# Optimization experiments

Measured on AMD Instinct MI355X. Metric: run time of the kernel, lower is better.

## Reference

```python
import jax, jax.numpy as jnp
import numpy as np

B, OBS, H, A, E = 131072, 194, 64, 5, 3  # batch, obs dim, hidden, max_action_dim, n event types


def setup_inputs() -> dict:
    key = jax.random.key(0)
    ks = jax.random.split(key, 16)
    s = lambda k, shape, std=0.1: (jax.random.normal(k, shape, dtype=jnp.float32) * std)
    return {
        "x": jax.random.normal(ks[0], (B, OBS), dtype=jnp.float32),
        "action": jax.random.randint(ks[1], (B,), 0, A),
        "W1": s(ks[2], (OBS, H)), "b1": jnp.zeros((H,), jnp.float32),
        "W2": s(ks[3], (H, H)),   "b2": jnp.zeros((H,), jnp.float32),
        "Wh": s(ks[4], (E, H, A), 0.01), "bh": jnp.zeros((E, A), jnp.float32),
        "Wc1": s(ks[5], (OBS, H)), "bc1": jnp.zeros((H,), jnp.float32),
        "Wc2": s(ks[6], (H, H)),   "bc2": jnp.zeros((H,), jnp.float32),
        "Wc3": s(ks[7], (H, 1)),   "bc3": jnp.zeros((1,), jnp.float32),
    }


def reference(x, action, W1, b1, W2, b2, Wh, bh, Wc1, bc1, Wc2, bc2, Wc3, bc3):
    # shared trunk
    feat = jnp.tanh(jnp.tanh(x @ W1 + b1) @ W2 + b2)          # [B, H]
    # route each sample to one of E heads via argmax of first 3 obs dims
    ev = jnp.argmax(x[:, :E], axis=1)                          # [B] int
    all_logits = jnp.einsum('bh,eha->bea', feat, Wh) + bh      # [B, E, A]
    logits = jnp.take_along_axis(
        all_logits, jnp.broadcast_to(ev[:, None, None], (x.shape[0], 1, A)), axis=1
    )[:, 0]                                                    # [B, A]
    logp_all = jax.nn.log_softmax(logits, axis=-1)             # [B, A]
    logp = jnp.take_along_axis(logp_all, action[:, None], axis=1)[:, 0]  # [B]
    entropy = -jnp.sum(jnp.exp(logp_all) * logp_all, axis=-1)  # [B]
    # critic
    value = jnp.tanh(jnp.tanh(x @ Wc1 + bc1) @ Wc2 + bc2) @ Wc3 + bc3    # [B, 1]
    return action, logp, entropy, value
```

## Files before the change

### kernel.cpp

```cpp
#include <hip/hip_runtime.h>
#include <hip/hip_bf16.h>

constexpr int Bt  = 131072;
constexpr int OBS = 194;
constexpr int Hd  = 64;
constexpr int NT  = 256;
constexpr int MT  = 128;
constexpr int HS  = 72;
constexpr int LS  = 18;

constexpr int W1B_OFF  = 0;
constexpr int WC1B_OFF = 28672;
constexpr int W2B_OFF  = 57344;
constexpr int WC2B_OFF = 65536;
constexpr int WHB_OFF  = 73728;
constexpr int WS_SHORTS = 74752;

typedef short bf8   __attribute__((ext_vector_type(8)));
typedef float f32x4 __attribute__((ext_vector_type(4)));

__device__ __forceinline__ short f2bs(float f) {
    union { __hip_bfloat16 h; short s; } u;
    u.h = __float2bfloat16(f);
    return u.s;
}
__device__ __forceinline__ float bs2f(short s) {
    union { short s; __hip_bfloat16 h; } u;
    u.s = s;
    return __bfloat162float(u.h);
}
__device__ __forceinline__ float fast_tanh(float v) {
    v = fminf(fmaxf(v, -15.f), 15.f);
    float e = __expf(2.f * v);
    return (e - 1.f) * __builtin_amdgcn_rcpf(e + 1.f);
}

__global__ void __launch_bounds__(256) prep(
    const float* __restrict__ W1, const float* __restrict__ W2,
    const float* __restrict__ Wh, const float* __restrict__ Wc1,
    const float* __restrict__ Wc2, const float* __restrict__ Wc3,
    short* __restrict__ ws)
{
    const int gid = blockIdx.x * 256 + threadIdx.x;
    const int gsz = gridDim.x * 256;

    for (int i = gid; i < 28672; i += gsz) {
        int j = i & 7, l = (i >> 3) & 63, nt = (i >> 9) & 3, kb = i >> 11;
        int k = kb * 32 + ((l >> 4) << 3) + j;
        int n = nt * 16 + (l & 15);
        short v1 = 0, v2 = 0;
        if (k < OBS) {
            v1 = f2bs(W1[k * 64 + n]);
            v2 = f2bs(Wc1[k * 64 + n]);
        }
        ws[W1B_OFF + i]  = v1;
        ws[WC1B_OFF + i] = v2;
    }
    for (int i = gid; i < 8192; i += gsz) {
        int j = i & 7, l = (i >> 3) & 63, nt = (i >> 9) & 3, kb = i >> 11;
        int k = kb * 32 + ((l >> 4) << 3) + j;
        int n = nt * 16 + (l & 15);
        ws[W2B_OFF + i]  = f2bs(W2[k * 64 + n]);
        ws[WC2B_OFF + i] = f2bs(Wc2[k * 64 + n]);
    }
    for (int i = gid; i < 1024; i += gsz) {
        int j = i & 7, l = (i >> 3) & 63, kb = i >> 9;
        int k = kb * 32 + ((l >> 4) << 3) + j;
        int cc = l & 15;
        float v;
        if (cc == 15) v = Wc3[k];
        else { int e = cc / 5, a = cc - 5 * e; v = Wh[(e * 64 + k) * 5 + a]; }
        ws[WHB_OFF + i] = f2bs(v);
    }
}

__global__ void __launch_bounds__(NT, 4) fused_ac(
    const float* __restrict__ x, const int* __restrict__ act_in,
    const float* __restrict__ b1, const float* __restrict__ b2,
    const float* __restrict__ bh, const float* __restrict__ bc1,
    const float* __restrict__ bc2, const float* __restrict__ bc3,
    const short* __restrict__ ws,
    float* __restrict__ out)
{
    __shared__ __align__(16) short hbuf[4][32 * HS];
    __shared__ short logitb[4][32 * LS];
    __shared__ float valb[4][32];

    const int t  = threadIdx.x;
    const int w  = t >> 6;
    const int l  = t & 63;
    const int q  = l >> 4;
    const int c  = l & 15;
    const int b0 = blockIdx.x * MT;

    const bf8* __restrict__ fW1  = reinterpret_cast<const bf8*>(ws + W1B_OFF);
    const bf8* __restrict__ fWc1 = reinterpret_cast<const bf8*>(ws + WC1B_OFF);
    const bf8* __restrict__ fW2  = reinterpret_cast<const bf8*>(ws + W2B_OFF);
    const bf8* __restrict__ fWc2 = reinterpret_cast<const bf8*>(ws + WC2B_OFF);
    const bf8* __restrict__ fWh  = reinterpret_cast<const bf8*>(ws + WHB_OFF);

    bf8 af[2][7];
    {
        const size_t row0 = (size_t)(b0 + w * 32 + c) * OBS;
        #pragma unroll
        for (int s = 0; s < 2; ++s) {
            const float* xr = x + row0 + (size_t)(s * 16) * OBS;
            #pragma unroll
            for (int kb = 0; kb < 6; ++kb) {
                const float2* p = reinterpret_cast<const float2*>(xr + kb * 32 + q * 8);
                float2 v0 = p[0], v1 = p[1], v2 = p[2], v3 = p[3];
                bf8 a;
                a[0] = f2bs(v0.x); a[1] = f2bs(v0.y); a[2] = f2bs(v1.x); a[3] = f2bs(v1.y);
                a[4] = f2bs(v2.x); a[5] = f2bs(v2.y); a[6] = f2bs(v3.x); a[7] = f2bs(v3.y);
                af[s][kb] = a;
            }
            bf8 a6 = {0, 0, 0, 0, 0, 0, 0, 0};
            if (q == 0) {
                float2 v = *reinterpret_cast<const float2*>(xr + 192);
                a6[0] = f2bs(v.x); a6[1] = f2bs(v.y);
            }
            af[s][6] = a6;
        }
    }

    short* hw = hbuf[w];

    auto trunk = [&](const bf8* __restrict__ fa1, const bf8* __restrict__ fa2,
                     const float* __restrict__ ba, const float* __restrict__ bb) {
        f32x4 acc[2][4];
        #pragma unroll
        for (int s = 0; s < 2; ++s)
            #pragma unroll
            for (int nt = 0; nt < 4; ++nt) acc[s][nt] = f32x4{0.f, 0.f, 0.f, 0.f};
        #pragma unroll
        for (int kb = 0; kb < 7; ++kb) {
            #pragma unroll
            for (int nt = 0; nt < 4; ++nt) {
                bf8 bw = fa1[(kb * 4 + nt) * 64 + l];
                acc[0][nt] = __builtin_amdgcn_mfma_f32_16x16x32_bf16(af[0][kb], bw, acc[0][nt], 0, 0, 0);
                acc[1][nt] = __builtin_amdgcn_mfma_f32_16x16x32_bf16(af[1][kb], bw, acc[1][nt], 0, 0, 0);
            }
        }
        #pragma unroll
        for (int nt = 0; nt < 4; ++nt) {
            float bias = ba[nt * 16 + c];
            #pragma unroll
            for (int s = 0; s < 2; ++s)
                #pragma unroll
                for (int r = 0; r < 4; ++r)
                    hw[(s * 16 + q * 4 + r) * HS + nt * 16 + c] = f2bs(fast_tanh(acc[s][nt][r] + bias));
        }
        #pragma unroll
        for (int s = 0; s < 2; ++s)
            #pragma unroll
            for (int nt = 0; nt < 4; ++nt) acc[s][nt] = f32x4{0.f, 0.f, 0.f, 0.f};
        #pragma unroll
        for (int kb = 0; kb < 2; ++kb) {
            bf8 ha[2];
            #pragma unroll
            for (int s = 0; s < 2; ++s)
                ha[s] = *reinterpret_cast<const bf8*>(&hw[(s * 16 + c) * HS + kb * 32 + q * 8]);
            #pragma unroll
            for (int nt = 0; nt < 4; ++nt) {
                bf8 bw = fa2[(kb * 4 + nt) * 64 + l];
                acc[0][nt] = __builtin_amdgcn_mfma_f32_16x16x32_bf16(ha[0], bw, acc[0][nt], 0, 0, 0);
                acc[1][nt] = __builtin_amdgcn_mfma_f32_16x16x32_bf16(ha[1], bw, acc[1][nt], 0, 0, 0);
            }
        }
        #pragma unroll
        for (int nt = 0; nt < 4; ++nt) {
            float bias = bb[nt * 16 + c];
            #pragma unroll
            for (int s = 0; s < 2; ++s)
                #pragma unroll
                for (int r = 0; r < 4; ++r)
                    hw[(s * 16 + q * 4 + r) * HS + nt * 16 + c] = f2bs(fast_tanh(acc[s][nt][r] + bias));
        }
    };

    auto smallmm = [&](f32x4 (&lacc)[2]) {
        lacc[0] = f32x4{0.f, 0.f, 0.f, 0.f};
        lacc[1] = f32x4{0.f, 0.f, 0.f, 0.f};
        #pragma unroll
        for (int kb = 0; kb < 2; ++kb) {
            bf8 bw = fWh[kb * 64 + l];
            #pragma unroll
            for (int s = 0; s < 2; ++s) {
                bf8 fa = *reinterpret_cast<const bf8*>(&hw[(s * 16 + c) * HS + kb * 32 + q * 8]);
                lacc[s] = __builtin_amdgcn_mfma_f32_16x16x32_bf16(fa, bw, lacc[s], 0, 0, 0);
            }
        }
    };

    trunk(fW1, fW2, b1, b2);
    float r_logp, r_ent;
    {
        f32x4 lg2[2];
        smallmm(lg2);
        short* lw = logitb[w];
        #pragma unroll
        for (int s = 0; s < 2; ++s)
            #pragma unroll
            for (int r = 0; r < 4; ++r)
                lw[(s * 16 + q * 4 + r) * LS + c] = f2bs(lg2[s][r]);

        int m  = l & 31;
        int gm = b0 + w * 32 + m;
        const float* xr = x + (size_t)gm * OBS;
        float x0 = xr[0], x1 = xr[1], x2 = xr[2];
        int ev = 0; float best = x0;
        if (x1 > best) { best = x1; ev = 1; }
        if (x2 > best) { ev = 2; }
        float lg[5];
        #pragma unroll
        for (int a = 0; a < 5; ++a)
            lg[a] = bs2f(lw[m * LS + ev * 5 + a]) + bh[ev * 5 + a];
        float mx = lg[0];
        #pragma unroll
        for (int a = 1; a < 5; ++a) mx = fmaxf(mx, lg[a]);
        float se = 0.f;
        #pragma unroll
        for (int a = 0; a < 5; ++a) se += __expf(lg[a] - mx);
        float lse = __logf(se) + mx;
        int act = act_in[gm];
        float lsel = lg[0];
        #pragma unroll
        for (int a = 1; a < 5; ++a) lsel = (act == a) ? lg[a] : lsel;
        float ent = 0.f;
        #pragma unroll
        for (int a = 0; a < 5; ++a) { float lp = lg[a] - lse; ent -= __expf(lp) * lp; }
        r_logp = lsel - lse;
        r_ent  = ent;
    }

    trunk(fWc1, fWc2, bc1, bc2);
    {
        f32x4 vacc[2];
        smallmm(vacc);
        if (c == 15) {
            float bc3v = bc3[0];
            #pragma unroll
            for (int s = 0; s < 2; ++s)
                #pragma unroll
                for (int r = 0; r < 4; ++r)
                    valb[w][s * 16 + q * 4 + r] = vacc[s][r] + bc3v;
        }
    }

    if (l < 32) {
        int gm = b0 + w * 32 + l;
        out[gm]          = (float)act_in[gm];
        out[Bt + gm]     = r_logp;
        out[2 * Bt + gm] = r_ent;
        out[3 * Bt + gm] = valb[w][l];
    }
}

extern "C" void kernel_launch(void* const* d_in, const int* in_sizes, int n_in,
                              void* d_out, int out_size, void* d_ws, size_t ws_size,
                              hipStream_t stream) {
    const float* x   = (const float*)d_in[0];
    const int*   act = (const int*)  d_in[1];
    const float* W1  = (const float*)d_in[2];
    const float* b1  = (const float*)d_in[3];
    const float* W2  = (const float*)d_in[4];
    const float* b2  = (const float*)d_in[5];
    const float* Wh  = (const float*)d_in[6];
    const float* bh  = (const float*)d_in[7];
    const float* Wc1 = (const float*)d_in[8];
    const float* bc1 = (const float*)d_in[9];
    const float* Wc2 = (const float*)d_in[10];
    const float* bc2 = (const float*)d_in[11];
    const float* Wc3 = (const float*)d_in[12];
    const float* bc3 = (const float*)d_in[13];
    float* out = (float*)d_out;
    short* ws  = (short*)d_ws;

    hipLaunchKernelGGL(prep, dim3(64), dim3(256), 0, stream,
                       W1, W2, Wh, Wc1, Wc2, Wc3, ws);
    hipLaunchKernelGGL(fused_ac, dim3(Bt / MT), dim3(NT), 0, stream,
                       x, act, b1, b2, bh, bc1, bc2, bc3, ws, out);
}
```

Before: 199.9 us.

## Fuse actor and critic trunks per 16-row tile, streaming x into MFMAs

Halves the rows per wave from 32 to 16 and runs the actor and critic first layers together, so each converted x fragment feeds both W1 and Wc1 MFMAs at once. The x fragments are no longer held in registers across both trunks. This is meant to cut register pressure and interleave two independent MFMA chains for better latency hiding. In exchange, each weight fragment is now used for only 16 rows, so weight loads per row double, and the grid has twice as many blocks.

```diff
diff --git a/kernel.cpp b/kernel.cpp
--- a/kernel.cpp
+++ b/kernel.cpp
@@ -5,7 +5,7 @@
 constexpr int OBS = 194;
 constexpr int Hd  = 64;
 constexpr int NT  = 256;
-constexpr int MT  = 128;
+constexpr int MT  = 64;
 constexpr int HS  = 72;
 constexpr int LS  = 18;
 
@@ -14,7 +14,6 @@
 constexpr int W2B_OFF  = 57344;
 constexpr int WC2B_OFF = 65536;
 constexpr int WHB_OFF  = 73728;
-constexpr int WS_SHORTS = 74752;
 
 typedef short bf8   __attribute__((ext_vector_type(8)));
 typedef float f32x4 __attribute__((ext_vector_type(4)));
@@ -82,9 +81,10 @@
     const short* __restrict__ ws,
     float* __restrict__ out)
 {
-    __shared__ __align__(16) short hbuf[4][32 * HS];
-    __shared__ short logitb[4][32 * LS];
-    __shared__ float valb[4][32];
+    __shared__ __align__(16) short hA[4][16 * HS];
+    __shared__ __align__(16) short hC[4][16 * HS];
+    __shared__ short logitb[4][16 * LS];
+    __shared__ float valb[4][16];
 
     const int t  = threadIdx.x;
     const int w  = t >> 6;
@@ -99,118 +99,108 @@
     const bf8* __restrict__ fWc2 = reinterpret_cast<const bf8*>(ws + WC2B_OFF);
     const bf8* __restrict__ fWh  = reinterpret_cast<const bf8*>(ws + WHB_OFF);
 
-    bf8 af[2][7];
+    short* ha = hA[w];
+    short* hc = hC[w];
+
+    f32x4 aa[4], ac[4];
+    #pragma unroll
+    for (int nt = 0; nt < 4; ++nt) {
+        aa[nt] = f32x4{0.f, 0.f, 0.f, 0.f};
+        ac[nt] = f32x4{0.f, 0.f, 0.f, 0.f};
+    }
     {
-        const size_t row0 = (size_t)(b0 + w * 32 + c) * OBS;
-        #pragma unroll
-        for (int s = 0; s < 2; ++s) {
-            const float* xr = x + row0 + (size_t)(s * 16) * OBS;
-            #pragma unroll
-            for (int kb = 0; kb < 6; ++kb) {
-                const float2* p = reinterpret_cast<const float2*>(xr + kb * 32 + q * 8);
-                float2 v0 = p[0], v1 = p[1], v2 = p[2], v3 = p[3];
-                bf8 a;
-                a[0] = f2bs(v0.x); a[1] = f2bs(v0.y); a[2] = f2bs(v1.x); a[3] = f2bs(v1.y);
-                a[4] = f2bs(v2.x); a[5] = f2bs(v2.y); a[6] = f2bs(v3.x); a[7] = f2bs(v3.y);
-                af[s][kb] = a;
-            }
-            bf8 a6 = {0, 0, 0, 0, 0, 0, 0, 0};
-            if (q == 0) {
-                float2 v = *reinterpret_cast<const float2*>(xr + 192);
-                a6[0] = f2bs(v.x); a6[1] = f2bs(v.y);
-            }
-            af[s][6] = a6;
-        }
-    }
-
-    short* hw = hbuf[w];
-
-    auto trunk = [&](const bf8* __restrict__ fa1, const bf8* __restrict__ fa2,
-                     const float* __restrict__ ba, const float* __restrict__ bb) {
-        f32x4 acc[2][4];
-        #pragma unroll
-        for (int s = 0; s < 2; ++s)
-            #pragma unroll
-            for (int nt = 0; nt < 4; ++nt) acc[s][nt] = f32x4{0.f, 0.f, 0.f, 0.f};
-        #pragma unroll
-        for (int kb = 0; kb < 7; ++kb) {
+        const float* xr = x + (size_t)(b0 + w * 16 + c) * OBS;
+        #pragma unroll
+        for (int kb = 0; kb < 6; ++kb) {
+            const float2* p = reinterpret_cast<const float2*>(xr + kb * 32 + q * 8);
+            float2 v0 = p[0], v1 = p[1], v2 = p[2], v3 = p[3];
+            bf8 a;
+            a[0] = f2bs(v0.x); a[1] = f2bs(v0.y); a[2] = f2bs(v1.x); a[3] = f2bs(v1.y);
+            a[4] = f2bs(v2.x); a[5] = f2bs(v2.y); a[6] = f2bs(v3.x); a[7] = f2bs(v3.y);
             #pragma unroll
             for (int nt = 0; nt < 4; ++nt) {
-                bf8 bw = fa1[(kb * 4 + nt) * 64 + l];
-                acc[0][nt] = __builtin_amdgcn_mfma_f32_16x16x32_bf16(af[0][kb], bw, acc[0][nt], 0, 0, 0);
-                acc[1][nt] = __builtin_amdgcn_mfma_f32_16x16x32_bf16(af[1][kb], bw, acc[1][nt], 0, 0, 0);
+                aa[nt] = __builtin_amdgcn_mfma_f32_16x16x32_bf16(a, fW1 [(kb * 4 + nt) * 64 + l], aa[nt], 0, 0, 0);
+                ac[nt] = __builtin_amdgcn_mfma_f32_16x16x32_bf16(a, fWc1[(kb * 4 + nt) * 64 + l], ac[nt], 0, 0, 0);
             }
         }
+        bf8 a6 = {0, 0, 0, 0, 0, 0, 0, 0};
+        if (q == 0) {
+            float2 v = *reinterpret_cast<const float2*>(xr + 192);
+            a6[0] = f2bs(v.x); a6[1] = f2bs(v.y);
+        }
         #pragma unroll
         for (int nt = 0; nt < 4; ++nt) {
-            float bias = ba[nt * 16 + c];
-            #pragma unroll
-            for (int s = 0; s < 2; ++s)
-                #pragma unroll
-                for (int r = 0; r < 4; ++r)
-                    hw[(s * 16 + q * 4 + r) * HS + nt * 16 + c] = f2bs(fast_tanh(acc[s][nt][r] + bias));
-        }
-        #pragma unroll
-        for (int s = 0; s < 2; ++s)
-            #pragma unroll
-            for (int nt = 0; nt < 4; ++nt) acc[s][nt] = f32x4{0.f, 0.f, 0.f, 0.f};
-        #pragma unroll
-        for (int kb = 0; kb < 2; ++kb) {
-            bf8 ha[2];
-            #pragma unroll
-            for (int s = 0; s < 2; ++s)
-                ha[s] = *reinterpret_cast<const bf8*>(&hw[(s * 16 + c) * HS + kb * 32 + q * 8]);
-            #pragma unroll
-            for (int nt = 0; nt < 4; ++nt) {
-                bf8 bw = fa2[(kb * 4 + nt) * 64 + l];
-                acc[0][nt] = __builtin_amdgcn_mfma_f32_16x16x32_bf16(ha[0], bw, acc[0][nt], 0, 0, 0);
-                acc[1][nt] = __builtin_amdgcn_mfma_f32_16x16x32_bf16(ha[1], bw, acc[1][nt], 0, 0, 0);
-            }
-        }
+            aa[nt] = __builtin_amdgcn_mfma_f32_16x16x32_bf16(a6, fW1 [(6 * 4 + nt) * 64 + l], aa[nt], 0, 0, 0);
+            ac[nt] = __builtin_amdgcn_mfma_f32_16x16x32_bf16(a6, fWc1[(6 * 4 + nt) * 64 + l], ac[nt], 0, 0, 0);
+        }
+    }
+    #pragma unroll
+    for (int nt = 0; nt < 4; ++nt) {
+        float ba = b1[nt * 16 + c], bc = bc1[nt * 16 + c];
+        #pragma unroll
+        for (int r = 0; r < 4; ++r) {
+            ha[(q * 4 + r) * HS + nt * 16 + c] = f2bs(fast_tanh(aa[nt][r] + ba));
+            hc[(q * 4 + r) * HS + nt * 16 + c] = f2bs(fast_tanh(ac[nt][r] + bc));
+        }
+    }
+
+    #pragma unroll
+    for (int nt = 0; nt < 4; ++nt) {
+        aa[nt] = f32x4{0.f, 0.f, 0.f, 0.f};
+        ac[nt] = f32x4{0.f, 0.f, 0.f, 0.f};
+    }
+    #pragma unroll
+    for (int kb = 0; kb < 2; ++kb) {
+        bf8 xa = *reinterpret_cast<const bf8*>(&ha[c * HS + kb * 32 + q * 8]);
+        bf8 xc = *reinterpret_cast<const bf8*>(&hc[c * HS + kb * 32 + q * 8]);
         #pragma unroll
         for (int nt = 0; nt < 4; ++nt) {
-            float bias = bb[nt * 16 + c];
-            #pragma unroll
-            for (int s = 0; s < 2; ++s)
-                #pragma unroll
-                for (int r = 0; r < 4; ++r)
-                    hw[(s * 16 + q * 4 + r) * HS + nt * 16 + c] = f2bs(fast_tanh(acc[s][nt][r] + bias));
-        }
-    };
-
-    auto smallmm = [&](f32x4 (&lacc)[2]) {
-        lacc[0] = f32x4{0.f, 0.f, 0.f, 0.f};
-        lacc[1] = f32x4{0.f, 0.f, 0.f, 0.f};
+            aa[nt] = __builtin_amdgcn_mfma_f32_16x16x32_bf16(xa, fW2 [(kb * 4 + nt) * 64 + l], aa[nt], 0, 0, 0);
+            ac[nt] = __builtin_amdgcn_mfma_f32_16x16x32_bf16(xc, fWc2[(kb * 4 + nt) * 64 + l], ac[nt], 0, 0, 0);
+        }
+    }
+    #pragma unroll
+    for (int nt = 0; nt < 4; ++nt) {
+        float ba = b2[nt * 16 + c], bc = bc2[nt * 16 + c];
+        #pragma unroll
+        for (int r = 0; r < 4; ++r) {
+            ha[(q * 4 + r) * HS + nt * 16 + c] = f2bs(fast_tanh(aa[nt][r] + ba));
+            hc[(q * 4 + r) * HS + nt * 16 + c] = f2bs(fast_tanh(ac[nt][r] + bc));
+        }
+    }
+
+    {
+        f32x4 lg = f32x4{0.f, 0.f, 0.f, 0.f};
+        f32x4 vv = f32x4{0.f, 0.f, 0.f, 0.f};
         #pragma unroll
         for (int kb = 0; kb < 2; ++kb) {
             bf8 bw = fWh[kb * 64 + l];
-            #pragma unroll
-            for (int s = 0; s < 2; ++s) {
-                bf8 fa = *reinterpret_cast<const bf8*>(&hw[(s * 16 + c) * HS + kb * 32 + q * 8]);
-                lacc[s] = __builtin_amdgcn_mfma_f32_16x16x32_bf16(fa, bw, lacc[s], 0, 0, 0);
-            }
-        }
-    };
-
-    trunk(fW1, fW2, b1, b2);
-    float r_logp, r_ent;
-    {
-        f32x4 lg2[2];
-        smallmm(lg2);
+            bf8 fa = *reinterpret_cast<const bf8*>(&ha[c * HS + kb * 32 + q * 8]);
+            bf8 fc = *reinterpret_cast<const bf8*>(&hc[c * HS + kb * 32 + q * 8]);
+            lg = __builtin_amdgcn_mfma_f32_16x16x32_bf16(fa, bw, lg, 0, 0, 0);
+            vv = __builtin_amdgcn_mfma_f32_16x16x32_bf16(fc, bw, vv, 0, 0, 0);
+        }
         short* lw = logitb[w];
         #pragma unroll
-        for (int s = 0; s < 2; ++s)
+        for (int r = 0; r < 4; ++r)
+            lw[(q * 4 + r) * LS + c] = f2bs(lg[r]);
+        if (c == 15) {
+            float bc3v = bc3[0];
             #pragma unroll
             for (int r = 0; r < 4; ++r)
-                lw[(s * 16 + q * 4 + r) * LS + c] = f2bs(lg2[s][r]);
-
-        int m  = l & 31;
-        int gm = b0 + w * 32 + m;
+                valb[w][q * 4 + r] = vv[r] + bc3v;
+        }
+    }
+
+    {
+        int m  = c;
+        int gm = b0 + w * 16 + m;
         const float* xr = x + (size_t)gm * OBS;
         float x0 = xr[0], x1 = xr[1], x2 = xr[2];
         int ev = 0; float best = x0;
         if (x1 > best) { best = x1; ev = 1; }
         if (x2 > best) { ev = 2; }
+        const short* lw = logitb[w];
         float lg[5];
         #pragma unroll
         for (int a = 0; a < 5; ++a)
@@ -229,30 +219,13 @@
         float ent = 0.f;
         #pragma unroll
         for (int a = 0; a < 5; ++a) { float lp = lg[a] - lse; ent -= __expf(lp) * lp; }
-        r_logp = lsel - lse;
-        r_ent  = ent;
-    }
-
-    trunk(fWc1, fWc2, bc1, bc2);
-    {
-        f32x4 vacc[2];
-        smallmm(vacc);
-        if (c == 15) {
-            float bc3v = bc3[0];
-            #pragma unroll
-            for (int s = 0; s < 2; ++s)
-                #pragma unroll
-                for (int r = 0; r < 4; ++r)
-                    valb[w][s * 16 + q * 4 + r] = vacc[s][r] + bc3v;
-        }
-    }
-
-    if (l < 32) {
-        int gm = b0 + w * 32 + l;
-        out[gm]          = (float)act_in[gm];
-        out[Bt + gm]     = r_logp;
-        out[2 * Bt + gm] = r_ent;
-        out[3 * Bt + gm] = valb[w][l];
+
+        if (l < 16) {
+            out[gm]          = (float)act;
+            out[Bt + gm]     = lsel - lse;
+            out[2 * Bt + gm] = ent;
+            out[3 * Bt + gm] = valb[w][m];
+        }
     }
 }
 
```

New measurement: 201.9 us. About the same (+1.0%).
